# Optimization experiments

Hardware: AMD Instinct MI355X
Metric: run time of the kernel (lower is better)

Reference implementation:

```python
import jax, jax.numpy as jnp
import numpy as np

B, H, M, R, DH = 4, 16, 2048, 32, 64
ROPE_BASE = 10000.0
NEG = -1e30  # finite stand-in for -inf masking


def setup_inputs() -> dict:
    key = jax.random.key(0)
    ks = jax.random.split(key, 9)
    s = 0.1
    inp = {
        'Pq': jax.random.normal(ks[0], (B, H, M, R), jnp.float32) * s,
        'Pk': jax.random.normal(ks[1], (B, H, M, R), jnp.float32) * s,
        'Pv': jax.random.normal(ks[2], (B, H, M, R), jnp.float32) * s,
        'Vq': jax.random.normal(ks[3], (H, R, DH), jnp.float32) * s,
        'Vk': jax.random.normal(ks[4], (H, R, DH), jnp.float32) * s,
        'Vv': jax.random.normal(ks[5], (H, R, DH), jnp.float32) * s,
        'bq': jax.random.normal(ks[6], (H * DH,), jnp.float32) * s,
        'bk': jax.random.normal(ks[7], (H * DH,), jnp.float32) * s,
        'bv': jax.random.normal(ks[8], (H * DH,), jnp.float32) * s,
        'attention_mask': jnp.ones((B, M), jnp.int32),
        'position_ids': jnp.broadcast_to(jnp.arange(M, dtype=jnp.int32)[None, :], (B, M)),
    }
    return inp


def _rope_half(x, c, s):
    # kernel semantics: split dh into halves, rotate with SAME cos/sin for both halves
    h = x.shape[-1] // 2
    x0, x1 = x[..., :h], x[..., h:]
    return jnp.concatenate([x0 * c - x1 * s, x0 * s + x1 * c], axis=-1)


def reference(Pq, Pk, Pv, Vq, Vk, Vv, bq, bk, bv, attention_mask, position_ids):
    Bs, Hs, Ms, Rs = Pq.shape
    dh = Vq.shape[-1]
    # --- cos/sin exactly as _build_cos_sin_bmd: interleaved duplication, kernel reads first dh/2 ---
    inv_freq = 1.0 / (ROPE_BASE ** (jnp.arange(0, dh, 2, dtype=jnp.float32) / dh))  # [dh/2]
    ang = position_ids.astype(jnp.float32)[..., None] * inv_freq  # [B,M,dh/2]
    ang_i = jnp.repeat(ang, 2, axis=-1)[..., : dh // 2]  # [c0,c0,c1,c1,...] first half
    cos = jnp.cos(ang_i)[:, None]  # [B,1,M,dh/2]
    sin = jnp.sin(ang_i)[:, None]
    # --- low-rank reconstruction of Q/K/V (+ flat per-head biases) ---
    Q = jnp.einsum('bhmr,hrd->bhmd', Pq, Vq) + bq.reshape(Hs, 1, dh)
    K = jnp.einsum('bhmr,hrd->bhmd', Pk, Vk) + bk.reshape(Hs, 1, dh)
    V = jnp.einsum('bhmr,hrd->bhmd', Pv, Vv) + bv.reshape(Hs, 1, dh)
    # --- inline RoPE ---
    Qr = _rope_half(Q, cos, sin)
    Kr = _rope_half(K, cos, sin)
    # --- attention: causal + pad mask, stable softmax ---
    scale = 1.0 / jnp.sqrt(jnp.float32(dh))
    scores = jnp.einsum('bhmd,bhnd->bhmn', Qr, Kr) * scale
    causal = jnp.tril(jnp.ones((Ms, Ms), dtype=bool))
    mask = causal[None, None, :, :] & (attention_mask > 0)[:, None, None, :]
    scores = jnp.where(mask, scores, NEG)
    p = jax.nn.softmax(scores, axis=-1)
    # kernel zeroes fully-masked rows (l_i == 0)
    any_valid = mask.any(axis=-1, keepdims=True)
    p = jnp.where(any_valid, p, 0.0)
    O = jnp.einsum('bhmn,bhnd->bhmd', p, V)
    return O.transpose(0, 2, 1, 3)  # [B,M,H,dh]
```

## Files before the change

kernel.cpp:

```cpp
#include <hip/hip_runtime.h>
#include <math.h>


#define B_ 4
#define H_ 16
#define M_ 2048
#define R_ 32
#define DH_ 64
#define BH_ 64
#define NEGV -1.0e30f
#define LOG2E 1.4426950408889634f

typedef float  f32x4  __attribute__((ext_vector_type(4)));
typedef __bf16 bf16x8 __attribute__((ext_vector_type(8)));
typedef unsigned short u16x4 __attribute__((ext_vector_type(4)));
typedef unsigned short u16x8 __attribute__((ext_vector_type(8)));

__device__ __forceinline__ unsigned short bfbits(float f) {
    __bf16 h = (__bf16)f;
    return __builtin_bit_cast(unsigned short, h);
}

__global__ void prep_kernel(const int* __restrict__ pid,
                            const float* __restrict__ Vq,
                            const float* __restrict__ Vk,
                            const float* __restrict__ Vv,
                            float* __restrict__ tab,
                            unsigned short* __restrict__ VTb)
{
    const int idx = blockIdx.x * 256 + threadIdx.x;
    if (idx < B_ * M_ * 16) {
        const int bm = idx >> 4, fi = idx & 15;
        const float invf = powf(10000.0f, -(float)fi * (1.0f / 32.0f));
        const float ang  = (float)pid[bm] * invf;
        float s, c;
        sincosf(ang, &s, &c);
        tab[(size_t)bm * 32 + fi]      = c;
        tab[(size_t)bm * 32 + 16 + fi] = s;
    } else {
        const int k = idx - B_ * M_ * 16;
        const float* src = (k < 32768) ? Vq : ((k < 65536) ? Vk : Vv);
        const int rem = k & 32767;
        const int h = rem >> 11, d = (rem >> 5) & 63, r = rem & 31;
        VTb[k] = bfbits(src[(h * 32 + r) * 64 + d]);
    }
}

__global__ __launch_bounds__(256) void qkv_proj_mfma_kernel(
    const float* __restrict__ Pq, const float* __restrict__ Pk,
    const float* __restrict__ Pv,
    const unsigned short* __restrict__ VTb,
    const float* __restrict__ bq, const float* __restrict__ bk,
    const float* __restrict__ bv,
    const float* __restrict__ tab,
    unsigned short* __restrict__ Qb, unsigned short* __restrict__ Kb,
    unsigned short* __restrict__ Vt)
{
    __shared__ unsigned short Ps[128 * 40];

    const int mat = blockIdx.z, bh = blockIdx.y, m0 = blockIdx.x * 128;
    const int h = bh & (H_ - 1), b = bh >> 4;
    const int t = threadIdx.x, w = t >> 6, lane = t & 63;
    const int c16 = lane & 15, g = lane >> 4, g8 = g << 3;

    const float* P    = (mat == 0) ? Pq : ((mat == 1) ? Pk : Pv);
    const float* bias = (mat == 0) ? bq : ((mat == 1) ? bk : bv);
    const float scl = (mat == 0) ? 0.125f * LOG2E : 1.0f;

    const float* Pg = P + ((size_t)bh * M_ + m0) * 32;
    #pragma unroll
    for (int pass = 0; pass < 4; ++pass) {
        const int lin = pass * 256 + t;
        const int row = lin >> 3, c4 = (lin & 7) << 2;
        const f32x4 v = *(const f32x4*)&Pg[row * 32 + c4];
        u16x4 b4;
        #pragma unroll
        for (int e = 0; e < 4; ++e) b4[e] = bfbits(v[e]);
        *(u16x4*)&Ps[row * 40 + c4] = b4;
    }

    bf16x8 vf[4];
    #pragma unroll
    for (int di = 0; di < 4; ++di)
        vf[di] = *(const bf16x8*)&VTb[((size_t)((mat * 16 + h) * 64 + di * 16 + c16)) * 32 + g8];

    __syncthreads();

    bf16x8 af[2];
    #pragma unroll
    for (int mi = 0; mi < 2; ++mi)
        af[mi] = *(const bf16x8*)&Ps[(w * 32 + mi * 16 + c16) * 40 + g8];

    f32x4 acc[2][4];
    const f32x4 z4 = {0.f, 0.f, 0.f, 0.f};
    #pragma unroll
    for (int mi = 0; mi < 2; ++mi)
        #pragma unroll
        for (int di = 0; di < 4; ++di)
            acc[mi][di] = __builtin_amdgcn_mfma_f32_16x16x32_bf16(af[mi], vf[di], z4, 0, 0, 0);

    float bsv[4];
    #pragma unroll
    for (int di = 0; di < 4; ++di) bsv[di] = bias[h * 64 + di * 16 + c16];

    if (mat == 2) {
        #pragma unroll
        for (int di = 0; di < 4; ++di) {
            u16x8 v8;
            #pragma unroll
            for (int mi = 0; mi < 2; ++mi)
                #pragma unroll
                for (int reg = 0; reg < 4; ++reg)
                    v8[(mi << 2) | reg] = bfbits(acc[mi][di][reg] + bsv[di]);
            const int d = di * 16 + c16;
            *(u16x8*)&Vt[((size_t)(bh * 64 + d)) * M_ + m0 + w * 32 + g8] = v8;
        }
    } else {
        unsigned short* Out = (mat == 0) ? Qb : Kb;
        #pragma unroll
        for (int mi = 0; mi < 2; ++mi)
            #pragma unroll
            for (int reg = 0; reg < 4; ++reg) {
                const int m = m0 + w * 32 + mi * 16 + (g << 2) + reg;
                const float x0 = acc[mi][0][reg] + bsv[0];
                const float x1 = acc[mi][1][reg] + bsv[1];
                const float x2 = acc[mi][2][reg] + bsv[2];
                const float x3 = acc[mi][3][reg] + bsv[3];
                const size_t o = ((size_t)bh * M_ + m) * 64;
                const size_t bm = (size_t)b * M_ + m;
                const int fi = c16 >> 1;
                const float c0 = tab[bm * 32 + fi],     s0 = tab[bm * 32 + 16 + fi];
                const float c1 = tab[bm * 32 + 8 + fi], s1 = tab[bm * 32 + 24 + fi];
                Out[o + c16]      = bfbits((x0 * c0 - x2 * s0) * scl);
                Out[o + 16 + c16] = bfbits((x1 * c1 - x3 * s1) * scl);
                Out[o + 32 + c16] = bfbits((x0 * s0 + x2 * c0) * scl);
                Out[o + 48 + c16] = bfbits((x1 * s1 + x3 * c1) * scl);
            }
    }
}

__global__ __launch_bounds__(256, 4) void flash_mfma_kernel(
    const unsigned short* __restrict__ Qus, const unsigned short* __restrict__ Kus,
    const unsigned short* __restrict__ Vtus, const int* __restrict__ amask,
    float* __restrict__ out)
{
    __shared__ unsigned short Ks[64 * 72];
    __shared__ unsigned short Vts[64 * 72];
    __shared__ int ams[64];

    const int bid = blockIdx.x;
    const int xcd = bid & 7, loc = bid >> 3;
    const int bh  = xcd * 8 + (loc & 7);
    const int px  = loc >> 3;
    const int h = bh & (H_ - 1), b = bh >> 4;
    const int t = threadIdx.x;
    const int w = t >> 6, lane = t & 63;
    const int c16 = lane & 15, g = lane >> 4;
    const int g4 = g << 2, g8 = g << 3;
    const int w16 = w << 4;
    const int srow = t >> 2, sc0 = (t & 3) << 4;

    const unsigned short* Kg  = Kus  + (size_t)bh * M_ * 64;
    const unsigned short* Vtg = Vtus + (size_t)bh * 64 * M_;
    const f32x4 zero4 = {0.f, 0.f, 0.f, 0.f};

    bf16x8 onesf;
    #pragma unroll
    for (int e = 0; e < 8; ++e) onesf[e] = (__bf16)1.0f;

    for (int pick = 0; pick < 2; ++pick) {
        const int qt = pick ? px : (31 - px);
        const int q0 = qt << 6;
        const int nkt = qt + 1;

        bf16x8 qf[2];
        #pragma unroll
        for (int kkd = 0; kkd < 2; ++kkd)
            qf[kkd] = *(const bf16x8*)(Qus +
                ((size_t)bh * M_ + q0 + w16 + c16) * 64 + kkd * 32 + g8);
        const int qrow = q0 + w16 + c16;

        f32x4 oT[4];
        #pragma unroll
        for (int di = 0; di < 4; ++di) oT[di] = zero4;
        f32x4 lacc = zero4;
        float mr = -3.0e38f;

        u16x8 kreg0, kreg1, vreg0, vreg1;
        int amreg = 0;
        {
            const unsigned short* gk = Kg + (size_t)srow * 64 + sc0;
            kreg0 = *(const u16x8*)gk; kreg1 = *(const u16x8*)(gk + 8);
            const unsigned short* gv = Vtg + (size_t)srow * M_ + sc0;
            vreg0 = *(const u16x8*)gv; vreg1 = *(const u16x8*)(gv + 8);
            if (t < 64) amreg = amask[b * M_ + t];
        }

        for (int kt = 0; kt < nkt; ++kt) {
            const int n0 = kt << 6;
            __syncthreads();
            *(u16x8*)&Ks[srow * 72 + sc0]      = kreg0;
            *(u16x8*)&Ks[srow * 72 + sc0 + 8]  = kreg1;
            *(u16x8*)&Vts[srow * 72 + sc0]     = vreg0;
            *(u16x8*)&Vts[srow * 72 + sc0 + 8] = vreg1;
            if (t < 64) ams[t] = amreg;
            __syncthreads();

            if (kt + 1 < nkt) {
                const int n1 = n0 + 64;
                const unsigned short* gk = Kg + (size_t)(n1 + srow) * 64 + sc0;
                kreg0 = *(const u16x8*)gk; kreg1 = *(const u16x8*)(gk + 8);
                const unsigned short* gv = Vtg + (size_t)srow * M_ + n1 + sc0;
                vreg0 = *(const u16x8*)gv; vreg1 = *(const u16x8*)(gv + 8);
                if (t < 64) amreg = amask[b * M_ + n1 + t];
            }

            f32x4 st[4];
            #pragma unroll
            for (int ni = 0; ni < 4; ++ni) st[ni] = zero4;
            __builtin_amdgcn_s_setprio(1);
            #pragma unroll
            for (int kkd = 0; kkd < 2; ++kkd)
                #pragma unroll
                for (int ni = 0; ni < 4; ++ni) {
                    const bf16x8 kf = *(const bf16x8*)&Ks[(ni * 16 + c16) * 72 + kkd * 32 + g8];
                    st[ni] = __builtin_amdgcn_mfma_f32_16x16x32_bf16(kf, qf[kkd], st[ni], 0, 0, 0);
                }
            __builtin_amdgcn_s_setprio(0);

            const bool allv  = __all(ams[lane] > 0);
            const bool needc = (n0 + 63) > (q0 + w16);
            bf16x8 pf[2];
            {
                float tm = -3.0e38f;
                if (allv) {
                    if (needc) {
                        #pragma unroll
                        for (int ni = 0; ni < 4; ++ni)
                            #pragma unroll
                            for (int rg = 0; rg < 4; ++rg) {
                                const int n_loc = ni * 16 + g4 + rg;
                                const float sv = ((n0 + n_loc) <= qrow) ? st[ni][rg] : NEGV;
                                st[ni][rg] = sv;
                                tm = fmaxf(tm, sv);
                            }
                    } else {
                        #pragma unroll
                        for (int ni = 0; ni < 4; ++ni)
                            #pragma unroll
                            for (int rg = 0; rg < 4; ++rg)
                                tm = fmaxf(tm, st[ni][rg]);
                    }
                } else {
                    #pragma unroll
                    for (int ni = 0; ni < 4; ++ni)
                        #pragma unroll
                        for (int rg = 0; rg < 4; ++rg) {
                            const int n_loc = ni * 16 + g4 + rg;
                            const bool ok = ((n0 + n_loc) <= qrow) && (ams[n_loc] > 0);
                            const float sv = ok ? st[ni][rg] : NEGV;
                            st[ni][rg] = sv;
                            tm = fmaxf(tm, sv);
                        }
                }
                tm = fmaxf(tm, __shfl_xor(tm, 16));
                tm = fmaxf(tm, __shfl_xor(tm, 32));
                const bool skip = __all(tm <= mr + 7.0f);
                if (!skip) {
                    const float mnew  = fmaxf(mr, tm);
                    const float alpha = exp2f(mr - mnew);
                    mr = mnew;
                    #pragma unroll
                    for (int di = 0; di < 4; ++di)
                        #pragma unroll
                        for (int rg = 0; rg < 4; ++rg)
                            oT[di][rg] *= alpha;
                    lacc[0] *= alpha;
                }
                if (allv) {
                    #pragma unroll
                    for (int ni = 0; ni < 4; ++ni)
                        #pragma unroll
                        for (int rg = 0; rg < 4; ++rg)
                            pf[ni >> 1][((ni & 1) << 2) | rg] =
                                (__bf16)exp2f(st[ni][rg] - mr);
                } else {
                    #pragma unroll
                    for (int ni = 0; ni < 4; ++ni)
                        #pragma unroll
                        for (int rg = 0; rg < 4; ++rg) {
                            const float sv = st[ni][rg];
                            const float pv = (sv > -1.0e29f) ? exp2f(sv - mr) : 0.f;
                            pf[ni >> 1][((ni & 1) << 2) | rg] = (__bf16)pv;
                        }
                }
            }

            __builtin_amdgcn_s_setprio(1);
            lacc = __builtin_amdgcn_mfma_f32_16x16x32_bf16(onesf, pf[0], lacc, 0, 0, 0);
            lacc = __builtin_amdgcn_mfma_f32_16x16x32_bf16(onesf, pf[1], lacc, 0, 0, 0);
            #pragma unroll
            for (int di = 0; di < 4; ++di)
                #pragma unroll
                for (int kk = 0; kk < 2; ++kk) {
                    const bf16x8 vfr = *(const bf16x8*)&Vts[(di * 16 + c16) * 72 + kk * 32 + g8];
                    oT[di] = __builtin_amdgcn_mfma_f32_16x16x32_bf16(vfr, pf[kk], oT[di], 0, 0, 0);
                }
            __builtin_amdgcn_s_setprio(0);
        }

        const float inv = (lacc[0] > 0.f) ? 1.f / lacc[0] : 0.f;
        const int q = q0 + w16 + c16;
        #pragma unroll
        for (int di = 0; di < 4; ++di) {
            f32x4 ov;
            #pragma unroll
            for (int rg = 0; rg < 4; ++rg) ov[rg] = oT[di][rg] * inv;
            *(f32x4*)&out[((size_t)(b * M_ + q) * H_ + h) * 64 + di * 16 + g4] = ov;
        }
    }
}

extern "C" void kernel_launch(void* const* d_in, const int* in_sizes, int n_in,
                              void* d_out, int out_size, void* d_ws, size_t ws_size,
                              hipStream_t stream)
{
    const float* Pq = (const float*)d_in[0];
    const float* Pk = (const float*)d_in[1];
    const float* Pv = (const float*)d_in[2];
    const float* Vq = (const float*)d_in[3];
    const float* Vk = (const float*)d_in[4];
    const float* Vv = (const float*)d_in[5];
    const float* bq = (const float*)d_in[6];
    const float* bk = (const float*)d_in[7];
    const float* bv = (const float*)d_in[8];
    const int*   am = (const int*)d_in[9];
    const int*   pid = (const int*)d_in[10];
    float* out = (float*)d_out;

    float* tab = (float*)d_ws;
    unsigned short* VTb = (unsigned short*)((char*)d_ws + (1 << 20));
    unsigned short* Qb  = (unsigned short*)((char*)d_ws + (2 << 20));
    unsigned short* Kb = Qb + (size_t)B_ * H_ * M_ * 64;
    unsigned short* Vt = Kb + (size_t)B_ * H_ * M_ * 64;

    prep_kernel<<<dim3((B_ * M_ * 16 + 98304) / 256), dim3(256), 0, stream>>>(
        pid, Vq, Vk, Vv, tab, VTb);

    qkv_proj_mfma_kernel<<<dim3(16, 64, 3), dim3(256), 0, stream>>>(
        Pq, Pk, Pv, VTb, bq, bk, bv, tab, Qb, Kb, Vt);

    flash_mfma_kernel<<<dim3(1024), dim3(256), 0, stream>>>(
        Qb, Kb, Vt, am, out);
}
```

Baseline: 200.2 us.

## Split flash blocks per query tile, stage RoPE table and outputs in LDS

The flash kernel now launches one block per query tile (2048 blocks) instead of pairing a long and short tile per block, and raises the launch-bounds occupancy hint from 4 to 8. The attention-mask value is kept in a register and read by shuffle instead of through shared memory. The projection kernel stages the cos/sin table in LDS and writes Q/K through an LDS buffer so global stores are coalesced 16-byte vectors. powf is replaced with exp2f. Unpaired causal tiles risk load imbalance, and the tighter occupancy hint may cause register spills.

After: 524.7 us. +162.0%, slower.

```diff
diff --git a/kernel.cpp b/kernel.cpp
--- a/kernel.cpp
+++ b/kernel.cpp
@@ -31,7 +31,7 @@
     const int idx = blockIdx.x * 256 + threadIdx.x;
     if (idx < B_ * M_ * 16) {
         const int bm = idx >> 4, fi = idx & 15;
-        const float invf = powf(10000.0f, -(float)fi * (1.0f / 32.0f));
+        const float invf = exp2f((float)fi * -0.4152410118609203f);
         const float ang  = (float)pid[bm] * invf;
         float s, c;
         sincosf(ang, &s, &c);
@@ -57,6 +57,8 @@
     unsigned short* __restrict__ Vt)
 {
     __shared__ unsigned short Ps[128 * 40];
+    __shared__ float Tabs[128 * 32];
+    __shared__ unsigned short Os[128 * 72];
 
     const int mat = blockIdx.z, bh = blockIdx.y, m0 = blockIdx.x * 128;
     const int h = bh & (H_ - 1), b = bh >> 4;
@@ -78,6 +80,14 @@
         for (int e = 0; e < 4; ++e) b4[e] = bfbits(v[e]);
         *(u16x4*)&Ps[row * 40 + c4] = b4;
     }
+    if (mat != 2) {
+        const float* tg = tab + ((size_t)b * M_ + m0) * 32;
+        #pragma unroll
+        for (int pass = 0; pass < 4; ++pass) {
+            const int lin = pass * 256 + t;
+            *(f32x4*)&Tabs[lin << 2] = *(const f32x4*)&tg[lin << 2];
+        }
+    }
 
     bf16x8 vf[4];
     #pragma unroll
@@ -115,43 +125,50 @@
             const int d = di * 16 + c16;
             *(u16x8*)&Vt[((size_t)(bh * 64 + d)) * M_ + m0 + w * 32 + g8] = v8;
         }
+        __syncthreads();
     } else {
-        unsigned short* Out = (mat == 0) ? Qb : Kb;
         #pragma unroll
         for (int mi = 0; mi < 2; ++mi)
             #pragma unroll
             for (int reg = 0; reg < 4; ++reg) {
-                const int m = m0 + w * 32 + mi * 16 + (g << 2) + reg;
+                const int mloc = w * 32 + mi * 16 + (g << 2) + reg;
                 const float x0 = acc[mi][0][reg] + bsv[0];
                 const float x1 = acc[mi][1][reg] + bsv[1];
                 const float x2 = acc[mi][2][reg] + bsv[2];
                 const float x3 = acc[mi][3][reg] + bsv[3];
-                const size_t o = ((size_t)bh * M_ + m) * 64;
-                const size_t bm = (size_t)b * M_ + m;
                 const int fi = c16 >> 1;
-                const float c0 = tab[bm * 32 + fi],     s0 = tab[bm * 32 + 16 + fi];
-                const float c1 = tab[bm * 32 + 8 + fi], s1 = tab[bm * 32 + 24 + fi];
-                Out[o + c16]      = bfbits((x0 * c0 - x2 * s0) * scl);
-                Out[o + 16 + c16] = bfbits((x1 * c1 - x3 * s1) * scl);
-                Out[o + 32 + c16] = bfbits((x0 * s0 + x2 * c0) * scl);
-                Out[o + 48 + c16] = bfbits((x1 * s1 + x3 * c1) * scl);
-            }
-    }
-}
-
-__global__ __launch_bounds__(256, 4) void flash_mfma_kernel(
+                const float c0 = Tabs[mloc * 32 + fi],     s0 = Tabs[mloc * 32 + 16 + fi];
+                const float c1 = Tabs[mloc * 32 + 8 + fi], s1 = Tabs[mloc * 32 + 24 + fi];
+                Os[mloc * 72 + c16]      = bfbits((x0 * c0 - x2 * s0) * scl);
+                Os[mloc * 72 + 16 + c16] = bfbits((x1 * c1 - x3 * s1) * scl);
+                Os[mloc * 72 + 32 + c16] = bfbits((x0 * s0 + x2 * c0) * scl);
+                Os[mloc * 72 + 48 + c16] = bfbits((x1 * s1 + x3 * c1) * scl);
+            }
+        __syncthreads();
+        unsigned short* Outg = ((mat == 0) ? Qb : Kb) + ((size_t)bh * M_ + m0) * 64;
+        #pragma unroll
+        for (int pass = 0; pass < 4; ++pass) {
+            const int lin = pass * 256 + t;
+            const int row = lin >> 3, seg = lin & 7;
+            *(u16x8*)&Outg[row * 64 + seg * 8] = *(const u16x8*)&Os[row * 72 + seg * 8];
+        }
+    }
+}
+
+__global__ __launch_bounds__(256, 8) void flash_mfma_kernel(
     const unsigned short* __restrict__ Qus, const unsigned short* __restrict__ Kus,
     const unsigned short* __restrict__ Vtus, const int* __restrict__ amask,
     float* __restrict__ out)
 {
     __shared__ unsigned short Ks[64 * 72];
     __shared__ unsigned short Vts[64 * 72];
-    __shared__ int ams[64];
 
     const int bid = blockIdx.x;
     const int xcd = bid & 7, loc = bid >> 3;
     const int bh  = xcd * 8 + (loc & 7);
-    const int px  = loc >> 3;
+    const int qt  = 31 - (loc >> 3);
+    const int q0  = qt << 6;
+    const int nkt = qt + 1;
     const int h = bh & (H_ - 1), b = bh >> 4;
     const int t = threadIdx.x;
     const int w = t >> 6, lane = t & 63;
@@ -168,156 +185,150 @@
     #pragma unroll
     for (int e = 0; e < 8; ++e) onesf[e] = (__bf16)1.0f;
 
-    for (int pick = 0; pick < 2; ++pick) {
-        const int qt = pick ? px : (31 - px);
-        const int q0 = qt << 6;
-        const int nkt = qt + 1;
-
-        bf16x8 qf[2];
+    bf16x8 qf[2];
+    #pragma unroll
+    for (int kkd = 0; kkd < 2; ++kkd)
+        qf[kkd] = *(const bf16x8*)(Qus +
+            ((size_t)bh * M_ + q0 + w16 + c16) * 64 + kkd * 32 + g8);
+    const int qrow = q0 + w16 + c16;
+
+    f32x4 oT[4];
+    #pragma unroll
+    for (int di = 0; di < 4; ++di) oT[di] = zero4;
+    f32x4 lacc = zero4;
+    float mr = -3.0e38f;
+
+    u16x8 kreg0, kreg1, vreg0, vreg1;
+    int am_next;
+    {
+        const unsigned short* gk = Kg + (size_t)srow * 64 + sc0;
+        kreg0 = *(const u16x8*)gk; kreg1 = *(const u16x8*)(gk + 8);
+        const unsigned short* gv = Vtg + (size_t)srow * M_ + sc0;
+        vreg0 = *(const u16x8*)gv; vreg1 = *(const u16x8*)(gv + 8);
+        am_next = amask[b * M_ + lane];
+    }
+
+    for (int kt = 0; kt < nkt; ++kt) {
+        const int n0 = kt << 6;
+        const int am_cur = am_next;
+        __syncthreads();
+        *(u16x8*)&Ks[srow * 72 + sc0]      = kreg0;
+        *(u16x8*)&Ks[srow * 72 + sc0 + 8]  = kreg1;
+        *(u16x8*)&Vts[srow * 72 + sc0]     = vreg0;
+        *(u16x8*)&Vts[srow * 72 + sc0 + 8] = vreg1;
+        __syncthreads();
+
+        if (kt + 1 < nkt) {
+            const int n1 = n0 + 64;
+            const unsigned short* gk = Kg + (size_t)(n1 + srow) * 64 + sc0;
+            kreg0 = *(const u16x8*)gk; kreg1 = *(const u16x8*)(gk + 8);
+            const unsigned short* gv = Vtg + (size_t)srow * M_ + n1 + sc0;
+            vreg0 = *(const u16x8*)gv; vreg1 = *(const u16x8*)(gv + 8);
+            am_next = amask[b * M_ + n1 + lane];
+        }
+
+        f32x4 st[4];
+        #pragma unroll
+        for (int ni = 0; ni < 4; ++ni) st[ni] = zero4;
+        __builtin_amdgcn_s_setprio(1);
         #pragma unroll
         for (int kkd = 0; kkd < 2; ++kkd)
-            qf[kkd] = *(const bf16x8*)(Qus +
-                ((size_t)bh * M_ + q0 + w16 + c16) * 64 + kkd * 32 + g8);
-        const int qrow = q0 + w16 + c16;
-
-        f32x4 oT[4];
-        #pragma unroll
-        for (int di = 0; di < 4; ++di) oT[di] = zero4;
-        f32x4 lacc = zero4;
-        float mr = -3.0e38f;
-
-        u16x8 kreg0, kreg1, vreg0, vreg1;
-        int amreg = 0;
+            #pragma unroll
+            for (int ni = 0; ni < 4; ++ni) {
+                const bf16x8 kf = *(const bf16x8*)&Ks[(ni * 16 + c16) * 72 + kkd * 32 + g8];
+                st[ni] = __builtin_amdgcn_mfma_f32_16x16x32_bf16(kf, qf[kkd], st[ni], 0, 0, 0);
+            }
+        __builtin_amdgcn_s_setprio(0);
+
+        const bool allv  = __all(am_cur > 0);
+        const bool needc = (n0 + 63) > (q0 + w16);
+        bf16x8 pf[2];
         {
-            const unsigned short* gk = Kg + (size_t)srow * 64 + sc0;
-            kreg0 = *(const u16x8*)gk; kreg1 = *(const u16x8*)(gk + 8);
-            const unsigned short* gv = Vtg + (size_t)srow * M_ + sc0;
-            vreg0 = *(const u16x8*)gv; vreg1 = *(const u16x8*)(gv + 8);
-            if (t < 64) amreg = amask[b * M_ + t];
-        }
-
-        for (int kt = 0; kt < nkt; ++kt) {
-            const int n0 = kt << 6;
-            __syncthreads();
-            *(u16x8*)&Ks[srow * 72 + sc0]      = kreg0;
-            *(u16x8*)&Ks[srow * 72 + sc0 + 8]  = kreg1;
-            *(u16x8*)&Vts[srow * 72 + sc0]     = vreg0;
-            *(u16x8*)&Vts[srow * 72 + sc0 + 8] = vreg1;
-            if (t < 64) ams[t] = amreg;
-            __syncthreads();
-
-            if (kt + 1 < nkt) {
-                const int n1 = n0 + 64;
-                const unsigned short* gk = Kg + (size_t)(n1 + srow) * 64 + sc0;
-                kreg0 = *(const u16x8*)gk; kreg1 = *(const u16x8*)(gk + 8);
-                const unsigned short* gv = Vtg + (size_t)srow * M_ + n1 + sc0;
-                vreg0 = *(const u16x8*)gv; vreg1 = *(const u16x8*)(gv + 8);
-                if (t < 64) amreg = amask[b * M_ + n1 + t];
-            }
-
-            f32x4 st[4];
-            #pragma unroll
-            for (int ni = 0; ni < 4; ++ni) st[ni] = zero4;
-            __builtin_amdgcn_s_setprio(1);
-            #pragma unroll
-            for (int kkd = 0; kkd < 2; ++kkd)
-                #pragma unroll
-                for (int ni = 0; ni < 4; ++ni) {
-                    const bf16x8 kf = *(const bf16x8*)&Ks[(ni * 16 + c16) * 72 + kkd * 32 + g8];
-                    st[ni] = __builtin_amdgcn_mfma_f32_16x16x32_bf16(kf, qf[kkd], st[ni], 0, 0, 0);
-                }
-            __builtin_amdgcn_s_setprio(0);
-
-            const bool allv  = __all(ams[lane] > 0);
-            const bool needc = (n0 + 63) > (q0 + w16);
-            bf16x8 pf[2];
-            {
-                float tm = -3.0e38f;
-                if (allv) {
-                    if (needc) {
-                        #pragma unroll
-                        for (int ni = 0; ni < 4; ++ni)
-                            #pragma unroll
-                            for (int rg = 0; rg < 4; ++rg) {
-                                const int n_loc = ni * 16 + g4 + rg;
-                                const float sv = ((n0 + n_loc) <= qrow) ? st[ni][rg] : NEGV;
-                                st[ni][rg] = sv;
-                                tm = fmaxf(tm, sv);
-                            }
-                    } else {
-                        #pragma unroll
-                        for (int ni = 0; ni < 4; ++ni)
-                            #pragma unroll
-                            for (int rg = 0; rg < 4; ++rg)
-                                tm = fmaxf(tm, st[ni][rg]);
-                    }
-                } else {
+            float tm = -3.0e38f;
+            if (allv) {
+                if (needc) {
                     #pragma unroll
                     for (int ni = 0; ni < 4; ++ni)
                         #pragma unroll
                         for (int rg = 0; rg < 4; ++rg) {
                             const int n_loc = ni * 16 + g4 + rg;
-                            const bool ok = ((n0 + n_loc) <= qrow) && (ams[n_loc] > 0);
-                            const float sv = ok ? st[ni][rg] : NEGV;
+                            const float sv = ((n0 + n_loc) <= qrow) ? st[ni][rg] : NEGV;
                             st[ni][rg] = sv;
                             tm = fmaxf(tm, sv);
                         }
-                }
-                tm = fmaxf(tm, __shfl_xor(tm, 16));
-                tm = fmaxf(tm, __shfl_xor(tm, 32));
-                const bool skip = __all(tm <= mr + 7.0f);
-                if (!skip) {
-                    const float mnew  = fmaxf(mr, tm);
-                    const float alpha = exp2f(mr - mnew);
-                    mr = mnew;
-                    #pragma unroll
-                    for (int di = 0; di < 4; ++di)
-                        #pragma unroll
-                        for (int rg = 0; rg < 4; ++rg)
-                            oT[di][rg] *= alpha;
-                    lacc[0] *= alpha;
-                }
-                if (allv) {
+                } else {
                     #pragma unroll
                     for (int ni = 0; ni < 4; ++ni)
                         #pragma unroll
                         for (int rg = 0; rg < 4; ++rg)
-                            pf[ni >> 1][((ni & 1) << 2) | rg] =
-                                (__bf16)exp2f(st[ni][rg] - mr);
-                } else {
-                    #pragma unroll
-                    for (int ni = 0; ni < 4; ++ni)
-                        #pragma unroll
-                        for (int rg = 0; rg < 4; ++rg) {
-                            const float sv = st[ni][rg];
-                            const float pv = (sv > -1.0e29f) ? exp2f(sv - mr) : 0.f;
-                            pf[ni >> 1][((ni & 1) << 2) | rg] = (__bf16)pv;
-                        }
+                            tm = fmaxf(tm, st[ni][rg]);
                 }
-            }
-
-            __builtin_amdgcn_s_setprio(1);
-            lacc = __builtin_amdgcn_mfma_f32_16x16x32_bf16(onesf, pf[0], lacc, 0, 0, 0);
-            lacc = __builtin_amdgcn_mfma_f32_16x16x32_bf16(onesf, pf[1], lacc, 0, 0, 0);
+            } else {
+                #pragma unroll
+                for (int ni = 0; ni < 4; ++ni)
+                    #pragma unroll
+                    for (int rg = 0; rg < 4; ++rg) {
+                        const int n_loc = ni * 16 + g4 + rg;
+                        const bool ok = ((n0 + n_loc) <= qrow) && (__shfl(am_cur, n_loc) > 0);
+                        const float sv = ok ? st[ni][rg] : NEGV;
+                        st[ni][rg] = sv;
+                        tm = fmaxf(tm, sv);
+                    }
+            }
+            tm = fmaxf(tm, __shfl_xor(tm, 16));
+            tm = fmaxf(tm, __shfl_xor(tm, 32));
+            const bool skip = __all(tm <= mr + 7.0f);
+            if (!skip) {
+                const float mnew  = fmaxf(mr, tm);
+                const float alpha = exp2f(mr - mnew);
+                mr = mnew;
+                #pragma unroll
+                for (int di = 0; di < 4; ++di)
+                    #pragma unroll
+                    for (int rg = 0; rg < 4; ++rg)
+                        oT[di][rg] *= alpha;
+                lacc[0] *= alpha;
+            }
+            if (allv) {
+                #pragma unroll
+                for (int ni = 0; ni < 4; ++ni)
+                    #pragma unroll
+                    for (int rg = 0; rg < 4; ++rg)
+                        pf[ni >> 1][((ni & 1) << 2) | rg] =
+                            (__bf16)exp2f(st[ni][rg] - mr);
+            } else {
+                #pragma unroll
+                for (int ni = 0; ni < 4; ++ni)
+                    #pragma unroll
+                    for (int rg = 0; rg < 4; ++rg) {
+                        const float sv = st[ni][rg];
+                        const float pv = (sv > -1.0e29f) ? exp2f(sv - mr) : 0.f;
+                        pf[ni >> 1][((ni & 1) << 2) | rg] = (__bf16)pv;
+                    }
+            }
+        }
+
+        __builtin_amdgcn_s_setprio(1);
+        lacc = __builtin_amdgcn_mfma_f32_16x16x32_bf16(onesf, pf[0], lacc, 0, 0, 0);
+        lacc = __builtin_amdgcn_mfma_f32_16x16x32_bf16(onesf, pf[1], lacc, 0, 0, 0);
+        #pragma unroll
+        for (int di = 0; di < 4; ++di)
             #pragma unroll
-            for (int di = 0; di < 4; ++di)
-                #pragma unroll
-                for (int kk = 0; kk < 2; ++kk) {
-                    const bf16x8 vfr = *(const bf16x8*)&Vts[(di * 16 + c16) * 72 + kk * 32 + g8];
-                    oT[di] = __builtin_amdgcn_mfma_f32_16x16x32_bf16(vfr, pf[kk], oT[di], 0, 0, 0);
-                }
-            __builtin_amdgcn_s_setprio(0);
-        }
-
-        const float inv = (lacc[0] > 0.f) ? 1.f / lacc[0] : 0.f;
-        const int q = q0 + w16 + c16;
-        #pragma unroll
-        for (int di = 0; di < 4; ++di) {
-            f32x4 ov;
-            #pragma unroll
-            for (int rg = 0; rg < 4; ++rg) ov[rg] = oT[di][rg] * inv;
-            *(f32x4*)&out[((size_t)(b * M_ + q) * H_ + h) * 64 + di * 16 + g4] = ov;
-        }
+            for (int kk = 0; kk < 2; ++kk) {
+                const bf16x8 vfr = *(const bf16x8*)&Vts[(di * 16 + c16) * 72 + kk * 32 + g8];
+                oT[di] = __builtin_amdgcn_mfma_f32_16x16x32_bf16(vfr, pf[kk], oT[di], 0, 0, 0);
+            }
+        __builtin_amdgcn_s_setprio(0);
+    }
+
+    const float inv = (lacc[0] > 0.f) ? 1.f / lacc[0] : 0.f;
+    const int q = q0 + w16 + c16;
+    #pragma unroll
+    for (int di = 0; di < 4; ++di) {
+        f32x4 ov;
+        #pragma unroll
+        for (int rg = 0; rg < 4; ++rg) ov[rg] = oT[di][rg] * inv;
+        *(f32x4*)&out[((size_t)(b * M_ + q) * H_ + h) * 64 + di * 16 + g4] = ov;
     }
 }
 
@@ -350,6 +361,6 @@
     qkv_proj_mfma_kernel<<<dim3(16, 64, 3), dim3(256), 0, stream>>>(
         Pq, Pk, Pv, VTb, bq, bk, bv, tab, Qb, Kb, Vt);
 
-    flash_mfma_kernel<<<dim3(1024), dim3(256), 0, stream>>>(
+    flash_mfma_kernel<<<dim3(2048), dim3(256), 0, stream>>>(
         Qb, Kb, Vt, am, out);
 }
```
